# Optimization experiments

Hardware: AMD Instinct MI355X
Metric: run time of the kernel (lower is better)

Reference implementation:

```python
import jax, jax.numpy as jnp
import numpy as np

N_DEST, N_SRC = 8192, 8192
FEAT, TFD, EMB, HID, HEADS = 1024, 256, 64, 128, 2
NEG_INF = -9e15


def setup_inputs() -> dict:
    key = jax.random.key(0)
    ks = jax.random.split(key, 8)
    bias = (jax.random.uniform(ks[0], (N_DEST, N_SRC)) < 0.01).astype(jnp.float32)
    emb_dest = jax.random.normal(ks[1], (N_DEST, EMB), jnp.float32)
    emb_src = jax.random.normal(ks[2], (N_SRC, EMB), jnp.float32)
    feature_src = jax.random.normal(ks[3], (N_SRC, FEAT), jnp.float32)
    scale = 0.05
    fc_W = jax.random.normal(ks[4], (TFD, FEAT), jnp.float32) * scale
    fc_b = jnp.zeros((TFD,), jnp.float32)
    dec_W = jax.random.normal(ks[5], (FEAT, TFD), jnp.float32) * scale
    dec_b = jnp.zeros((FEAT,), jnp.float32)
    att_W = jax.random.normal(ks[6], (HEADS, EMB, HID), jnp.float32) * scale
    att_W2 = jax.random.normal(ks[7], (HEADS, HID, HID), jnp.float32) * scale
    return dict(bias=bias, emb_dest=emb_dest, emb_src=emb_src,
                feature_src=feature_src, fc_W=fc_W, fc_b=fc_b,
                dec_W=dec_W, dec_b=dec_b, att_W=att_W, att_W2=att_W2)


def reference(bias, emb_dest, emb_src, feature_src, fc_W, fc_b, dec_W, dec_b, att_W, att_W2):
    # encoder: [N_src, FEAT] -> [N_src, TFD]
    transformed = feature_src @ fc_W.T + fc_b
    # per-head projections of node embeddings: h = emb @ W  -> [H, N, HID]
    h_src = jnp.einsum('ne,hed->hnd', emb_src, att_W)
    h_dst = jnp.einsum('me,hed->hmd', emb_dest, att_W)
    # e = elu((h_dst @ W2) @ h_src^T)  -> [H, N_dest, N_src]
    scores = jax.nn.elu(jnp.einsum('hmd,hdk,hnk->hmn', h_dst, att_W2, h_src))
    masked = jnp.where(bias > 0, scores, NEG_INF)
    attn = jax.nn.softmax(masked, axis=-1)  # row-wise over source nodes
    # aggregate transformed source features, mean over heads -> [N_dest, TFD]
    feature_src_re = jnp.einsum('hmn,nf->hmf', attn, transformed).mean(axis=0)
    # decoder (autoencoder reconstruction): [N_src, FEAT]
    feature_hat = transformed @ dec_W.T + dec_b
    return feature_src_re, feature_hat
```

## Files before the change

### kernel.cpp

```cpp
#include <hip/hip_runtime.h>
#include <hip/hip_bf16.h>

#define N_DEST 8192
#define N_SRC  8192
#define FEATD  1024
#define TFDIM  256
#define EMBD   64
#define HIDD   128
#define LDO    1024
#define CAP 1024
#define LSTRIDE 256
#define SCAP 240

typedef float  f32x4  __attribute__((ext_vector_type(4)));
typedef __bf16 bf16x8 __attribute__((ext_vector_type(8)));
typedef unsigned short u16x4 __attribute__((ext_vector_type(4)));

__device__ inline bf16x8 load8cvt(const float* p) {
  const f32x4 u = *(const f32x4*)p;
  const f32x4 v = *(const f32x4*)(p + 4);
  bf16x8 r;
  #pragma unroll
  for (int i = 0; i < 4; ++i) { r[i] = (__bf16)u[i]; r[i + 4] = (__bf16)v[i]; }
  return r;
}
__device__ inline unsigned short bfbits(float f) {
  __bf16 b = (__bf16)f;
  return *(unsigned short*)&b;
}
__device__ inline float bf2f(unsigned short u) {
  union { unsigned int i; float f; } x;
  x.i = (unsigned int)u << 16;
  return x.f;
}

__global__ __launch_bounds__(256) void gemm_mfma_k1(
    const float* __restrict__ A, const float* __restrict__ B,
    const float* __restrict__ bias, float* __restrict__ stage,
    unsigned short* __restrict__ apack)
{
  const int wave = threadIdx.x >> 6, lane = threadIdx.x & 63;
  const int l15 = lane & 15, quad = lane >> 4;
  const int row0 = blockIdx.x * 64 + wave * 16;
  const int col0 = blockIdx.y * 64;

  const float* Ap = A + (size_t)(row0 + l15) * FEATD + quad * 8;
  const float* Bp = B + (size_t)(col0 + l15) * FEATD + quad * 8;

  f32x4 acc[4];
  #pragma unroll
  for (int i = 0; i < 4; ++i) acc[i] = (f32x4){0.f, 0.f, 0.f, 0.f};

  for (int k = 0; k < FEATD; k += 32) {
    const bf16x8 a  = load8cvt(Ap + k);
    const bf16x8 b0 = load8cvt(Bp + k);
    const bf16x8 b1 = load8cvt(Bp + (size_t)16 * FEATD + k);
    const bf16x8 b2 = load8cvt(Bp + (size_t)32 * FEATD + k);
    const bf16x8 b3 = load8cvt(Bp + (size_t)48 * FEATD + k);
    acc[0] = __builtin_amdgcn_mfma_f32_16x16x32_bf16(a, b0, acc[0], 0, 0, 0);
    acc[1] = __builtin_amdgcn_mfma_f32_16x16x32_bf16(a, b1, acc[1], 0, 0, 0);
    acc[2] = __builtin_amdgcn_mfma_f32_16x16x32_bf16(a, b2, acc[2], 0, 0, 0);
    acc[3] = __builtin_amdgcn_mfma_f32_16x16x32_bf16(a, b3, acc[3], 0, 0, 0);
  }

  #pragma unroll
  for (int ct = 0; ct < 4; ++ct) {
    const int n = col0 + ct * 16 + l15;
    const float bn = bias[n];
    #pragma unroll
    for (int r = 0; r < 4; ++r) {
      const int mm = row0 + quad * 4 + r;
      const float v = acc[ct][r] + bn;
      const unsigned short pb = bfbits(v);
      stage[(size_t)mm * LDO + n] = v;
      ((unsigned short*)(stage + (size_t)mm * LDO + 768))[n] = pb;
      if (apack) apack[(size_t)mm * TFDIM + n] = pb;
    }
  }
}

__global__ __launch_bounds__(128) void proj_all(
    const float* __restrict__ emb_src, const float* __restrict__ emb_dest,
    const float* __restrict__ att_W, const float* __restrict__ att_W2,
    float* __restrict__ stage)
{
  const int t = threadIdx.x;
  const int b = blockIdx.x;
  const int rb    = b & 511;
  const int h     = (b >> 9) & 1;
  const int which = b >> 10;
  const int row0  = rb * 16;

  __shared__ float se[16][EMBD];
  __shared__ float hh[16][HIDD];

  const float* e = (which ? emb_dest : emb_src) + (size_t)row0 * EMBD;
  for (int i = t; i < 16 * EMBD; i += 128) se[i >> 6][i & 63] = e[i];
  __syncthreads();

  float acc[16];
  #pragma unroll
  for (int r = 0; r < 16; ++r) acc[r] = 0.f;
  const float* W = att_W + (size_t)h * EMBD * HIDD + t;
  for (int d = 0; d < EMBD; ++d) {
    const float w = W[d * HIDD];
    #pragma unroll
    for (int r = 0; r < 16; ++r) acc[r] += se[r][d] * w;
  }

  if (!which) {
    #pragma unroll
    for (int r = 0; r < 16; ++r) {
      const size_t row = row0 + r;
      stage[row * LDO + 256 + h * HIDD + t] = acc[r];
      ((unsigned short*)(stage + row * LDO + 896))[h * HIDD + t] = bfbits(acc[r]);
    }
    return;
  }

  #pragma unroll
  for (int r = 0; r < 16; ++r) hh[r][t] = acc[r];
  __syncthreads();

  float g[16];
  #pragma unroll
  for (int r = 0; r < 16; ++r) g[r] = 0.f;
  const float* W2 = att_W2 + (size_t)h * HIDD * HIDD + t;
  for (int d = 0; d < HIDD; ++d) {
    const float w2 = W2[d * HIDD];
    #pragma unroll
    for (int r = 0; r < 16; ++r) g[r] += hh[r][d] * w2;
  }
  #pragma unroll
  for (int r = 0; r < 16; ++r)
    stage[(size_t)(row0 + r) * LDO + 512 + h * HIDD + t] = g[r];
}

__global__ __launch_bounds__(256) void extract_nbrs(
    const float* __restrict__ bias, int* __restrict__ counts,
    int* __restrict__ lists)
{
  const int m = blockIdx.x;
  __shared__ int cnt;
  __shared__ int buf[CAP];
  if (threadIdx.x == 0) cnt = 0;
  __syncthreads();
  const float* brow = bias + (size_t)m * N_SRC;
  for (int base = threadIdx.x * 4; base < N_SRC; base += 1024) {
    const f32x4 v = *(const f32x4*)(brow + base);
    #pragma unroll
    for (int e = 0; e < 4; ++e)
      if (v[e] > 0.f) {
        const int p = atomicAdd(&cnt, 1);
        if (p < CAP) buf[p] = base + e;
      }
  }
  __syncthreads();
  const int c = cnt;
  if (threadIdx.x == 0) counts[m] = c;
  int lim = c < LSTRIDE ? c : LSTRIDE;
  for (int t = threadIdx.x; t < lim; t += 256)
    lists[(size_t)m * LSTRIDE + t] = buf[t];
}

__global__ __launch_bounds__(256, 4) void attn_gather(
    const float* __restrict__ bias, const float* __restrict__ stage,
    const int* __restrict__ counts, const int* __restrict__ lists,
    float* __restrict__ out)
{
  const int m = blockIdx.x;
  const int tid = threadIdx.x;
  const int lane = tid & 63, wv = tid >> 6;

  __shared__ float g0[HIDD], g1[HIDD];
  __shared__ float s0[256], s1[256];
  __shared__ int   lidx[256];
  __shared__ float rA[4], rB[4];
  __shared__ float p0[4][TFDIM], p1[4][TFDIM];

  const float* gs = stage + (size_t)m * LDO + 512;
  if (tid < 128) { g0[tid] = gs[tid]; g1[tid] = gs[HIDD + tid]; }
  const int count = counts[m];
  __syncthreads();

  if (count > 0 && count <= SCAP) {
    const int countPad = (count + 15) & ~15;
    if (tid < countPad)
      lidx[tid] = (tid < count) ? lists[(size_t)m * LSTRIDE + tid] : 0;
    __syncthreads();

    const int grp = tid >> 3, r8 = tid & 7;
    for (int t0 = 0; t0 < count; t0 += 32) {
      const int t = t0 + grp;
      float q0 = 0.f, q1 = 0.f;
      if (t < count) {
        const int j = lidx[t];
        const __bf16* hb = (const __bf16*)(stage + (size_t)j * LDO + 896);
        const bf16x8 x0 = *(const bf16x8*)(hb + r8 * 16);
        const bf16x8 x1 = *(const bf16x8*)(hb + r8 * 16 + 8);
        const bf16x8 y0 = *(const bf16x8*)(hb + HIDD + r8 * 16);
        const bf16x8 y1 = *(const bf16x8*)(hb + HIDD + r8 * 16 + 8);
        #pragma unroll
        for (int e = 0; e < 8; ++e) {
          q0 += g0[r8 * 16 + e]     * (float)x0[e];
          q0 += g0[r8 * 16 + 8 + e] * (float)x1[e];
          q1 += g1[r8 * 16 + e]     * (float)y0[e];
          q1 += g1[r8 * 16 + 8 + e] * (float)y1[e];
        }
      }
      #pragma unroll
      for (int off = 1; off < 8; off <<= 1) {
        q0 += __shfl_xor(q0, off);
        q1 += __shfl_xor(q1, off);
      }
      if (r8 == 0 && t < count) {
        s0[t] = (q0 > 0.f) ? q0 : expm1f(q0);
        s1[t] = (q1 > 0.f) ? q1 : expm1f(q1);
      }
    }
    __syncthreads();

    float m0 = (tid < count) ? s0[tid] : -3.4e38f;
    float m1 = (tid < count) ? s1[tid] : -3.4e38f;
    #pragma unroll
    for (int off = 32; off; off >>= 1) {
      m0 = fmaxf(m0, __shfl_xor(m0, off));
      m1 = fmaxf(m1, __shfl_xor(m1, off));
    }
    if (lane == 0) { rA[wv] = m0; rB[wv] = m1; }
    __syncthreads();
    const float M0 = fmaxf(fmaxf(rA[0], rA[1]), fmaxf(rA[2], rA[3]));
    const float M1 = fmaxf(fmaxf(rB[0], rB[1]), fmaxf(rB[2], rB[3]));
    __syncthreads();

    float w0 = 0.f, w1 = 0.f;
    if (tid < count) {
      w0 = __expf(s0[tid] - M0);
      w1 = __expf(s1[tid] - M1);
    }
    if (tid < countPad) { s0[tid] = w0; s1[tid] = w1; }
    float l0 = w0, l1 = w1;
    #pragma unroll
    for (int off = 32; off; off >>= 1) {
      l0 += __shfl_xor(l0, off);
      l1 += __shfl_xor(l1, off);
    }
    if (lane == 0) { rA[wv] = l0; rB[wv] = l1; }
    __syncthreads();
    const float L0 = rA[0] + rA[1] + rA[2] + rA[3];
    const float L1 = rB[0] + rB[1] + rB[2] + rB[3];

    float b0[4] = {0.f, 0.f, 0.f, 0.f};
    float b1[4] = {0.f, 0.f, 0.f, 0.f};
    const int c4 = lane << 2;
    for (int t = wv << 2; t < countPad; t += 16) {
      #pragma unroll
      for (int q = 0; q < 4; ++q) {
        const int j = lidx[t + q];
        const float u0 = s0[t + q], u1 = s1[t + q];
        const u16x4 tv = *(const u16x4*)(
            (const unsigned short*)(stage + (size_t)j * LDO + 768) + c4);
        #pragma unroll
        for (int i = 0; i < 4; ++i) {
          const float f = bf2f(tv[i]);
          b0[i] += u0 * f;
          b1[i] += u1 * f;
        }
      }
    }
    #pragma unroll
    for (int i = 0; i < 4; ++i) {
      p0[wv][c4 + i] = b0[i];
      p1[wv][c4 + i] = b1[i];
    }
    __syncthreads();
    const float A0 = p0[0][tid] + p0[1][tid] + p0[2][tid] + p0[3][tid];
    const float A1 = p1[0][tid] + p1[1][tid] + p1[2][tid] + p1[3][tid];
    out[(size_t)m * TFDIM + tid] = 0.5f * (A0 / L0 + A1 / L1);
    return;
  }

  float* w0s = (float*)p0[0];
  float* w1s = (float*)p0[1];
  const int c = tid;
  float a0 = 0.f, a1 = 0.f;
  float M0 = -3.4e38f, M1 = -3.4e38f, L0 = 0.f, L1 = 0.f;
  for (int j0 = 0; j0 < N_SRC; j0 += 256) {
    const int j = j0 + tid;
    const float* hb = stage + (size_t)j * LDO + 256;
    float q0 = 0.f, q1 = 0.f;
    for (int d = 0; d < HIDD; d += 4) {
      const f32x4 x = *(const f32x4*)(hb + d);
      const f32x4 y = *(const f32x4*)(hb + HIDD + d);
      #pragma unroll
      for (int e = 0; e < 4; ++e) {
        q0 += g0[d + e] * x[e];
        q1 += g1[d + e] * y[e];
      }
    }
    const bool nz = bias[(size_t)m * N_SRC + j] > 0.f;
    const float sc0 = nz ? ((q0 > 0.f) ? q0 : expm1f(q0)) : -9e15f;
    const float sc1 = nz ? ((q1 > 0.f) ? q1 : expm1f(q1)) : -9e15f;

    float cm0 = sc0, cm1 = sc1;
    #pragma unroll
    for (int off = 32; off; off >>= 1) {
      cm0 = fmaxf(cm0, __shfl_xor(cm0, off));
      cm1 = fmaxf(cm1, __shfl_xor(cm1, off));
    }
    if (lane == 0) { rA[wv] = cm0; rB[wv] = cm1; }
    __syncthreads();
    const float CM0 = fmaxf(fmaxf(rA[0], rA[1]), fmaxf(rA[2], rA[3]));
    const float CM1 = fmaxf(fmaxf(rB[0], rB[1]), fmaxf(rB[2], rB[3]));
    __syncthreads();

    const float nM0 = fmaxf(M0, CM0), nM1 = fmaxf(M1, CM1);
    const float r0 = __expf(M0 - nM0), r1 = __expf(M1 - nM1);
    const float w0 = __expf(sc0 - nM0), w1 = __expf(sc1 - nM1);
    w0s[tid] = w0; w1s[tid] = w1;
    float cl0 = w0, cl1 = w1;
    #pragma unroll
    for (int off = 32; off; off >>= 1) {
      cl0 += __shfl_xor(cl0, off);
      cl1 += __shfl_xor(cl1, off);
    }
    if (lane == 0) { rA[wv] = cl0; rB[wv] = cl1; }
    __syncthreads();
    L0 = L0 * r0 + (rA[0] + rA[1] + rA[2] + rA[3]);
    L1 = L1 * r1 + (rB[0] + rB[1] + rB[2] + rB[3]);
    M0 = nM0; M1 = nM1;
    a0 *= r0; a1 *= r1;
    for (int t2 = 0; t2 < 256; ++t2) {
      const float tv = stage[(size_t)(j0 + t2) * LDO + c];
      a0 += w0s[t2] * tv;
      a1 += w1s[t2] * tv;
    }
    __syncthreads();
  }
  out[(size_t)m * TFDIM + c] = 0.5f * (a0 / L0 + a1 / L1);
}

__global__ __launch_bounds__(64) void attn_stream(
    const float* __restrict__ bias, const float* __restrict__ stage,
    float* __restrict__ out)
{
  const int lane = threadIdx.x;
  const int m = blockIdx.x;
  const int c0 = lane * 4;

  __shared__ float g0[HIDD], g1[HIDD];
  __shared__ int   ring[256];
  __shared__ float wb0[64], wb1[64];

  const float* gs = stage + (size_t)m * LDO + 512;
  g0[lane]      = gs[lane];
  g0[lane + 64] = gs[lane + 64];
  g1[lane]      = gs[HIDD + lane];
  g1[lane + 64] = gs[HIDD + lane + 64];
  __syncthreads();

  float O0[4] = {0.f, 0.f, 0.f, 0.f};
  float O1[4] = {0.f, 0.f, 0.f, 0.f};
  float M0 = -3.4e38f, M1 = -3.4e38f;
  float L0 = 0.f, L1 = 0.f;

  auto flush = [&](int b, int rp) {
    __syncthreads();
    int j = -1;
    if (lane < b) j = ring[(rp + lane) & 255];
    float s0 = 0.f, s1 = 0.f;
    if (j >= 0) {
      const float* h0 = stage + (size_t)j * LDO + 256;
      const float* h1 = h0 + HIDD;
      #pragma unroll
      for (int d = 0; d < HIDD; d += 4) {
        const f32x4 a = *(const f32x4*)(h0 + d);
        const f32x4 c = *(const f32x4*)(h1 + d);
        #pragma unroll
        for (int e = 0; e < 4; ++e) {
          s0 += g0[d + e] * a[e];
          s1 += g1[d + e] * c[e];
        }
      }
      s0 = (s0 > 0.f) ? s0 : expm1f(s0);
      s1 = (s1 > 0.f) ? s1 : expm1f(s1);
    }
    float m0 = (j >= 0) ? s0 : -3.4e38f;
    float m1 = (j >= 0) ? s1 : -3.4e38f;
    #pragma unroll
    for (int off = 32; off; off >>= 1) {
      m0 = fmaxf(m0, __shfl_xor(m0, off));
      m1 = fmaxf(m1, __shfl_xor(m1, off));
    }
    const float nM0 = fmaxf(M0, m0), nM1 = fmaxf(M1, m1);
    const float w0 = (j >= 0) ? __expf(s0 - nM0) : 0.f;
    const float w1 = (j >= 0) ? __expf(s1 - nM1) : 0.f;
    float l0 = w0, l1 = w1;
    #pragma unroll
    for (int off = 32; off; off >>= 1) {
      l0 += __shfl_xor(l0, off);
      l1 += __shfl_xor(l1, off);
    }
    const float r0 = __expf(M0 - nM0);
    const float r1 = __expf(M1 - nM1);
    L0 = L0 * r0 + l0;  L1 = L1 * r1 + l1;
    M0 = nM0;  M1 = nM1;
    #pragma unroll
    for (int i = 0; i < 4; ++i) { O0[i] *= r0; O1[i] *= r1; }
    wb0[lane] = w0;  wb1[lane] = w1;
    __syncthreads();
    for (int n = 0; n < b; ++n) {
      const int jj = ring[(rp + n) & 255];
      const float wa = wb0[n], wc = wb1[n];
      const f32x4 tv = *(const f32x4*)(stage + (size_t)jj * LDO + c0);
      #pragma unroll
      for (int i = 0; i < 4; ++i) {
        O0[i] += wa * tv[i];
        O1[i] += wc * tv[i];
      }
    }
    __syncthreads();
  };

  const float* brow = bias + (size_t)m * N_SRC;
  int wpos = 0, rpos = 0;
  for (int base = 0; base < N_SRC; base += 256) {
    const f32x4 v = *(const f32x4*)(brow + base + lane * 4);
    #pragma unroll
    for (int e = 0; e < 4; ++e) {
      const bool nz = v[e] > 0.f;
      const unsigned long long mask = __ballot(nz);
      if (nz) {
        const int pos = wpos + __popcll(mask & ((1ull << lane) - 1ull));
        ring[pos & 255] = base + lane * 4 + e;
      }
      wpos += __popcll(mask);
      if (wpos - rpos >= 64) { flush(64, rpos); rpos += 64; }
    }
  }
  while (wpos - rpos > 0) {
    const int b = (wpos - rpos < 64) ? (wpos - rpos) : 64;
    flush(b, rpos);
    rpos += b;
  }

  float* orow = out + (size_t)m * TFDIM + c0;
  if (wpos == 0) {
    float o[4] = {0.f, 0.f, 0.f, 0.f};
    for (int j = 0; j < N_SRC; ++j) {
      const f32x4 tv = *(const f32x4*)(stage + (size_t)j * LDO + c0);
      #pragma unroll
      for (int i = 0; i < 4; ++i) o[i] += tv[i];
    }
    const float inv = 1.f / (float)N_SRC;
    #pragma unroll
    for (int i = 0; i < 4; ++i) orow[i] = o[i] * inv;
  } else {
    const float i0 = 1.f / L0, i1 = 1.f / L1;
    #pragma unroll
    for (int i = 0; i < 4; ++i)
      orow[i] = 0.5f * (O0[i] * i0 + O1[i] * i1);
  }
}

__global__ __launch_bounds__(256) void gemm_mfma_dec2(
    const unsigned short* __restrict__ apack,
    const float* __restrict__ W,
    const float* __restrict__ bias,
    float* __restrict__ OUT)
{
  const int wave = threadIdx.x >> 6, lane = threadIdx.x & 63;
  const int l15 = lane & 15, quad = lane >> 4;
  const int row0 = blockIdx.x * 64 + wave * 16;
  const int col0 = blockIdx.y * 64;

  const unsigned short* Ap = apack + (size_t)(row0 + l15) * TFDIM + quad * 8;
  const float* Bp = W + (size_t)(col0 + l15) * TFDIM + quad * 8;

  f32x4 acc[4];
  #pragma unroll
  for (int i = 0; i < 4; ++i) acc[i] = (f32x4){0.f, 0.f, 0.f, 0.f};

  #pragma unroll
  for (int k = 0; k < TFDIM; k += 32) {
    const bf16x8 a  = *(const bf16x8*)(Ap + k);
    const bf16x8 b0 = load8cvt(Bp + k);
    const bf16x8 b1 = load8cvt(Bp + (size_t)16 * TFDIM + k);
    const bf16x8 b2 = load8cvt(Bp + (size_t)32 * TFDIM + k);
    const bf16x8 b3 = load8cvt(Bp + (size_t)48 * TFDIM + k);
    acc[0] = __builtin_amdgcn_mfma_f32_16x16x32_bf16(a, b0, acc[0], 0, 0, 0);
    acc[1] = __builtin_amdgcn_mfma_f32_16x16x32_bf16(a, b1, acc[1], 0, 0, 0);
    acc[2] = __builtin_amdgcn_mfma_f32_16x16x32_bf16(a, b2, acc[2], 0, 0, 0);
    acc[3] = __builtin_amdgcn_mfma_f32_16x16x32_bf16(a, b3, acc[3], 0, 0, 0);
  }

  #pragma unroll
  for (int ct = 0; ct < 4; ++ct) {
    const int n = col0 + ct * 16 + l15;
    const float bn = bias[n];
    #pragma unroll
    for (int r = 0; r < 4; ++r) {
      const int mm = row0 + quad * 4 + r;
      OUT[(size_t)mm * LDO + n] = acc[ct][r] + bn;
    }
  }
}

__global__ __launch_bounds__(128) void gemm_mfma_dec(
    const float* __restrict__ W,
    const float* __restrict__ bias,
    float* __restrict__ OUT)
{
  const int row0 = blockIdx.x * 32;
  const int tid = threadIdx.x;
  const int wave = tid >> 6, lane = tid & 63;
  const int l15 = lane & 15, quad = lane >> 4;

  __shared__ __bf16 Ab[32][TFDIM + 8];

  for (int i = tid; i < 32 * TFDIM; i += 128) {
    const int r = i >> 8, k = i & 255;
    Ab[r][k] = (__bf16)OUT[(size_t)(row0 + r) * LDO + k];
  }
  __syncthreads();

  bf16x8 af[8];
  #pragma unroll
  for (int ks = 0; ks < 8; ++ks)
    af[ks] = *(const bf16x8*)&Ab[wave * 16 + l15][ks * 32 + quad * 8];

  for (int ct = 0; ct < 16; ++ct) {
    f32x4 acc[4];
    #pragma unroll
    for (int i = 0; i < 4; ++i) acc[i] = (f32x4){0.f, 0.f, 0.f, 0.f};
    #pragma unroll
    for (int ks = 0; ks < 8; ++ks) {
      #pragma unroll
      for (int cg = 0; cg < 4; ++cg) {
        const int n = ct * 64 + cg * 16 + l15;
        const bf16x8 bf = load8cvt(W + (size_t)n * TFDIM + ks * 32 + quad * 8);
        acc[cg] = __builtin_amdgcn_mfma_f32_16x16x32_bf16(af[ks], bf, acc[cg], 0, 0, 0);
      }
    }
    #pragma unroll
    for (int cg = 0; cg < 4; ++cg) {
      const int n = ct * 64 + cg * 16 + l15;
      const float bn = bias[n];
      #pragma unroll
      for (int r = 0; r < 4; ++r) {
        const int mm = row0 + wave * 16 + quad * 4 + r;
        OUT[(size_t)mm * LDO + n] = acc[cg][r] + bn;
      }
    }
  }
}

extern "C" void kernel_launch(void* const* d_in, const int* in_sizes, int n_in,
                              void* d_out, int out_size, void* d_ws, size_t ws_size,
                              hipStream_t stream) {
  const float* bias        = (const float*)d_in[0];
  const float* emb_dest    = (const float*)d_in[1];
  const float* emb_src     = (const float*)d_in[2];
  const float* feature_src = (const float*)d_in[3];
  const float* fc_W        = (const float*)d_in[4];
  const float* fc_b        = (const float*)d_in[5];
  const float* dec_W       = (const float*)d_in[6];
  const float* dec_b       = (const float*)d_in[7];
  const float* att_W       = (const float*)d_in[8];
  const float* att_W2      = (const float*)d_in[9];

  float* out0 = (float*)d_out;
  float* out1 = out0 + (size_t)N_DEST * TFDIM;

  const size_t lists_bytes = (size_t)N_DEST * LSTRIDE * sizeof(int);
  const size_t apack_bytes = (size_t)N_SRC * TFDIM * sizeof(unsigned short);
  const size_t need = (size_t)65536 + lists_bytes + apack_bytes;
  const bool use_ws = (ws_size >= need);
  int* counts = (int*)d_ws;
  int* lists  = (int*)((char*)d_ws + 65536);
  unsigned short* apack =
      (unsigned short*)((char*)d_ws + 65536 + lists_bytes);

  {
    dim3 grid(N_SRC / 64, TFDIM / 64);
    gemm_mfma_k1<<<grid, 256, 0, stream>>>(feature_src, fc_W, fc_b, out1,
                                           use_ws ? apack : (unsigned short*)nullptr);
  }
  proj_all<<<2048, 128, 0, stream>>>(emb_src, emb_dest, att_W, att_W2, out1);
  if (use_ws) {
    extract_nbrs<<<N_DEST, 256, 0, stream>>>(bias, counts, lists);
    attn_gather<<<N_DEST, 256, 0, stream>>>(bias, out1, counts, lists, out0);
  } else {
    attn_stream<<<N_DEST, 64, 0, stream>>>(bias, out1, out0);
  }
  if (use_ws) {
    dim3 grid(N_SRC / 64, FEATD / 64);
    gemm_mfma_dec2<<<grid, 256, 0, stream>>>(apack, dec_W, dec_b, out1);
  } else {
    gemm_mfma_dec<<<N_SRC / 32, 128, 0, stream>>>(dec_W, dec_b, out1);
  }
}
```

Measured before the change: 692.3 us.

## Fuse neighbor extraction into attention kernel and pre-convert weights to bf16

Result: faster. 635.3 us (-8.2%).

```diff
diff --git a/kernel.cpp b/kernel.cpp
--- a/kernel.cpp
+++ b/kernel.cpp
@@ -8,8 +8,6 @@
 #define EMBD   64
 #define HIDD   128
 #define LDO    1024
-#define CAP 1024
-#define LSTRIDE 256
 #define SCAP 240
 
 typedef float  f32x4  __attribute__((ext_vector_type(4)));
@@ -34,10 +32,26 @@
   return x.f;
 }
 
+__global__ __launch_bounds__(256) void cvt_weights(
+    const float* __restrict__ fc_W, const float* __restrict__ dec_W,
+    unsigned short* __restrict__ wpack, unsigned short* __restrict__ dpack)
+{
+  const int which = blockIdx.x >> 8;
+  const int i = ((blockIdx.x & 255) * 256 + threadIdx.x) * 4;
+  const float* src = which ? dec_W : fc_W;
+  unsigned short* dst = which ? dpack : wpack;
+  const f32x4 v = *(const f32x4*)(src + i);
+  u16x4 o;
+  #pragma unroll
+  for (int e = 0; e < 4; ++e) o[e] = bfbits(v[e]);
+  *(u16x4*)(dst + i) = o;
+}
+
 __global__ __launch_bounds__(256) void gemm_mfma_k1(
     const float* __restrict__ A, const float* __restrict__ B,
     const float* __restrict__ bias, float* __restrict__ stage,
-    unsigned short* __restrict__ apack)
+    unsigned short* __restrict__ apack,
+    const unsigned short* __restrict__ wpack)
 {
   const int wave = threadIdx.x >> 6, lane = threadIdx.x & 63;
   const int l15 = lane & 15, quad = lane >> 4;
@@ -45,22 +59,37 @@
   const int col0 = blockIdx.y * 64;
 
   const float* Ap = A + (size_t)(row0 + l15) * FEATD + quad * 8;
-  const float* Bp = B + (size_t)(col0 + l15) * FEATD + quad * 8;
 
   f32x4 acc[4];
   #pragma unroll
   for (int i = 0; i < 4; ++i) acc[i] = (f32x4){0.f, 0.f, 0.f, 0.f};
 
-  for (int k = 0; k < FEATD; k += 32) {
-    const bf16x8 a  = load8cvt(Ap + k);
-    const bf16x8 b0 = load8cvt(Bp + k);
-    const bf16x8 b1 = load8cvt(Bp + (size_t)16 * FEATD + k);
-    const bf16x8 b2 = load8cvt(Bp + (size_t)32 * FEATD + k);
-    const bf16x8 b3 = load8cvt(Bp + (size_t)48 * FEATD + k);
-    acc[0] = __builtin_amdgcn_mfma_f32_16x16x32_bf16(a, b0, acc[0], 0, 0, 0);
-    acc[1] = __builtin_amdgcn_mfma_f32_16x16x32_bf16(a, b1, acc[1], 0, 0, 0);
-    acc[2] = __builtin_amdgcn_mfma_f32_16x16x32_bf16(a, b2, acc[2], 0, 0, 0);
-    acc[3] = __builtin_amdgcn_mfma_f32_16x16x32_bf16(a, b3, acc[3], 0, 0, 0);
+  if (wpack) {
+    const unsigned short* Bq = wpack + (size_t)(col0 + l15) * FEATD + quad * 8;
+    for (int k = 0; k < FEATD; k += 32) {
+      const bf16x8 a  = load8cvt(Ap + k);
+      const bf16x8 b0 = *(const bf16x8*)(Bq + k);
+      const bf16x8 b1 = *(const bf16x8*)(Bq + (size_t)16 * FEATD + k);
+      const bf16x8 b2 = *(const bf16x8*)(Bq + (size_t)32 * FEATD + k);
+      const bf16x8 b3 = *(const bf16x8*)(Bq + (size_t)48 * FEATD + k);
+      acc[0] = __builtin_amdgcn_mfma_f32_16x16x32_bf16(a, b0, acc[0], 0, 0, 0);
+      acc[1] = __builtin_amdgcn_mfma_f32_16x16x32_bf16(a, b1, acc[1], 0, 0, 0);
+      acc[2] = __builtin_amdgcn_mfma_f32_16x16x32_bf16(a, b2, acc[2], 0, 0, 0);
+      acc[3] = __builtin_amdgcn_mfma_f32_16x16x32_bf16(a, b3, acc[3], 0, 0, 0);
+    }
+  } else {
+    const float* Bp = B + (size_t)(col0 + l15) * FEATD + quad * 8;
+    for (int k = 0; k < FEATD; k += 32) {
+      const bf16x8 a  = load8cvt(Ap + k);
+      const bf16x8 b0 = load8cvt(Bp + k);
+      const bf16x8 b1 = load8cvt(Bp + (size_t)16 * FEATD + k);
+      const bf16x8 b2 = load8cvt(Bp + (size_t)32 * FEATD + k);
+      const bf16x8 b3 = load8cvt(Bp + (size_t)48 * FEATD + k);
+      acc[0] = __builtin_amdgcn_mfma_f32_16x16x32_bf16(a, b0, acc[0], 0, 0, 0);
+      acc[1] = __builtin_amdgcn_mfma_f32_16x16x32_bf16(a, b1, acc[1], 0, 0, 0);
+      acc[2] = __builtin_amdgcn_mfma_f32_16x16x32_bf16(a, b2, acc[2], 0, 0, 0);
+      acc[3] = __builtin_amdgcn_mfma_f32_16x16x32_bf16(a, b3, acc[3], 0, 0, 0);
+    }
   }
 
   #pragma unroll
@@ -136,36 +165,8 @@
     stage[(size_t)(row0 + r) * LDO + 512 + h * HIDD + t] = g[r];
 }
 
-__global__ __launch_bounds__(256) void extract_nbrs(
-    const float* __restrict__ bias, int* __restrict__ counts,
-    int* __restrict__ lists)
-{
-  const int m = blockIdx.x;
-  __shared__ int cnt;
-  __shared__ int buf[CAP];
-  if (threadIdx.x == 0) cnt = 0;
-  __syncthreads();
-  const float* brow = bias + (size_t)m * N_SRC;
-  for (int base = threadIdx.x * 4; base < N_SRC; base += 1024) {
-    const f32x4 v = *(const f32x4*)(brow + base);
-    #pragma unroll
-    for (int e = 0; e < 4; ++e)
-      if (v[e] > 0.f) {
-        const int p = atomicAdd(&cnt, 1);
-        if (p < CAP) buf[p] = base + e;
-      }
-  }
-  __syncthreads();
-  const int c = cnt;
-  if (threadIdx.x == 0) counts[m] = c;
-  int lim = c < LSTRIDE ? c : LSTRIDE;
-  for (int t = threadIdx.x; t < lim; t += 256)
-    lists[(size_t)m * LSTRIDE + t] = buf[t];
-}
-
-__global__ __launch_bounds__(256, 4) void attn_gather(
+__global__ __launch_bounds__(256, 4) void attn_fused(
     const float* __restrict__ bias, const float* __restrict__ stage,
-    const int* __restrict__ counts, const int* __restrict__ lists,
     float* __restrict__ out)
 {
   const int m = blockIdx.x;
@@ -177,45 +178,52 @@
   __shared__ int   lidx[256];
   __shared__ float rA[4], rB[4];
   __shared__ float p0[4][TFDIM], p1[4][TFDIM];
+  __shared__ int   cnt;
 
   const float* gs = stage + (size_t)m * LDO + 512;
   if (tid < 128) { g0[tid] = gs[tid]; g1[tid] = gs[HIDD + tid]; }
-  const int count = counts[m];
+  if (tid == 0) cnt = 0;
   __syncthreads();
+
+  const float* brow = bias + (size_t)m * N_SRC;
+  for (int base = tid * 4; base < N_SRC; base += 1024) {
+    const f32x4 v = *(const f32x4*)(brow + base);
+    #pragma unroll
+    for (int e = 0; e < 4; ++e)
+      if (v[e] > 0.f) {
+        const int p = atomicAdd(&cnt, 1);
+        if (p < 256) lidx[p] = base + e;
+      }
+  }
+  __syncthreads();
+  const int count = cnt;
 
   if (count > 0 && count <= SCAP) {
     const int countPad = (count + 15) & ~15;
-    if (tid < countPad)
-      lidx[tid] = (tid < count) ? lists[(size_t)m * LSTRIDE + tid] : 0;
-    __syncthreads();
-
-    const int grp = tid >> 3, r8 = tid & 7;
-    for (int t0 = 0; t0 < count; t0 += 32) {
+    if (tid >= count && tid < countPad) lidx[tid] = 0;
+    __syncthreads();
+
+    const int grp = tid >> 2, r4 = tid & 3;
+    const int h = r4 >> 1, half = r4 & 1;
+    const float* gh = (h ? g1 : g0) + half * 64;
+    for (int t0 = 0; t0 < count; t0 += 64) {
       const int t = t0 + grp;
-      float q0 = 0.f, q1 = 0.f;
+      float q = 0.f;
       if (t < count) {
         const int j = lidx[t];
-        const __bf16* hb = (const __bf16*)(stage + (size_t)j * LDO + 896);
-        const bf16x8 x0 = *(const bf16x8*)(hb + r8 * 16);
-        const bf16x8 x1 = *(const bf16x8*)(hb + r8 * 16 + 8);
-        const bf16x8 y0 = *(const bf16x8*)(hb + HIDD + r8 * 16);
-        const bf16x8 y1 = *(const bf16x8*)(hb + HIDD + r8 * 16 + 8);
+        const __bf16* hb =
+            (const __bf16*)(stage + (size_t)j * LDO + 896) + h * HIDD + half * 64;
         #pragma unroll
-        for (int e = 0; e < 8; ++e) {
-          q0 += g0[r8 * 16 + e]     * (float)x0[e];
-          q0 += g0[r8 * 16 + 8 + e] * (float)x1[e];
-          q1 += g1[r8 * 16 + e]     * (float)y0[e];
-          q1 += g1[r8 * 16 + 8 + e] * (float)y1[e];
+        for (int s = 0; s < 8; ++s) {
+          const bf16x8 x = *(const bf16x8*)(hb + s * 8);
+          #pragma unroll
+          for (int e = 0; e < 8; ++e) q += gh[s * 8 + e] * (float)x[e];
         }
       }
-      #pragma unroll
-      for (int off = 1; off < 8; off <<= 1) {
-        q0 += __shfl_xor(q0, off);
-        q1 += __shfl_xor(q1, off);
-      }
-      if (r8 == 0 && t < count) {
-        s0[t] = (q0 > 0.f) ? q0 : expm1f(q0);
-        s1[t] = (q1 > 0.f) ? q1 : expm1f(q1);
+      q += __shfl_xor(q, 1);
+      if (t < count && half == 0) {
+        const float sc = (q > 0.f) ? q : expm1f(q);
+        if (h == 0) s0[t] = sc; else s1[t] = sc;
       }
     }
     __syncthreads();
@@ -340,132 +348,9 @@
   out[(size_t)m * TFDIM + c] = 0.5f * (a0 / L0 + a1 / L1);
 }
 
-__global__ __launch_bounds__(64) void attn_stream(
-    const float* __restrict__ bias, const float* __restrict__ stage,
-    float* __restrict__ out)
-{
-  const int lane = threadIdx.x;
-  const int m = blockIdx.x;
-  const int c0 = lane * 4;
-
-  __shared__ float g0[HIDD], g1[HIDD];
-  __shared__ int   ring[256];
-  __shared__ float wb0[64], wb1[64];
-
-  const float* gs = stage + (size_t)m * LDO + 512;
-  g0[lane]      = gs[lane];
-  g0[lane + 64] = gs[lane + 64];
-  g1[lane]      = gs[HIDD + lane];
-  g1[lane + 64] = gs[HIDD + lane + 64];
-  __syncthreads();
-
-  float O0[4] = {0.f, 0.f, 0.f, 0.f};
-  float O1[4] = {0.f, 0.f, 0.f, 0.f};
-  float M0 = -3.4e38f, M1 = -3.4e38f;
-  float L0 = 0.f, L1 = 0.f;
-
-  auto flush = [&](int b, int rp) {
-    __syncthreads();
-    int j = -1;
-    if (lane < b) j = ring[(rp + lane) & 255];
-    float s0 = 0.f, s1 = 0.f;
-    if (j >= 0) {
-      const float* h0 = stage + (size_t)j * LDO + 256;
-      const float* h1 = h0 + HIDD;
-      #pragma unroll
-      for (int d = 0; d < HIDD; d += 4) {
-        const f32x4 a = *(const f32x4*)(h0 + d);
-        const f32x4 c = *(const f32x4*)(h1 + d);
-        #pragma unroll
-        for (int e = 0; e < 4; ++e) {
-          s0 += g0[d + e] * a[e];
-          s1 += g1[d + e] * c[e];
-        }
-      }
-      s0 = (s0 > 0.f) ? s0 : expm1f(s0);
-      s1 = (s1 > 0.f) ? s1 : expm1f(s1);
-    }
-    float m0 = (j >= 0) ? s0 : -3.4e38f;
-    float m1 = (j >= 0) ? s1 : -3.4e38f;
-    #pragma unroll
-    for (int off = 32; off; off >>= 1) {
-      m0 = fmaxf(m0, __shfl_xor(m0, off));
-      m1 = fmaxf(m1, __shfl_xor(m1, off));
-    }
-    const float nM0 = fmaxf(M0, m0), nM1 = fmaxf(M1, m1);
-    const float w0 = (j >= 0) ? __expf(s0 - nM0) : 0.f;
-    const float w1 = (j >= 0) ? __expf(s1 - nM1) : 0.f;
-    float l0 = w0, l1 = w1;
-    #pragma unroll
-    for (int off = 32; off; off >>= 1) {
-      l0 += __shfl_xor(l0, off);
-      l1 += __shfl_xor(l1, off);
-    }
-    const float r0 = __expf(M0 - nM0);
-    const float r1 = __expf(M1 - nM1);
-    L0 = L0 * r0 + l0;  L1 = L1 * r1 + l1;
-    M0 = nM0;  M1 = nM1;
-    #pragma unroll
-    for (int i = 0; i < 4; ++i) { O0[i] *= r0; O1[i] *= r1; }
-    wb0[lane] = w0;  wb1[lane] = w1;
-    __syncthreads();
-    for (int n = 0; n < b; ++n) {
-      const int jj = ring[(rp + n) & 255];
-      const float wa = wb0[n], wc = wb1[n];
-      const f32x4 tv = *(const f32x4*)(stage + (size_t)jj * LDO + c0);
-      #pragma unroll
-      for (int i = 0; i < 4; ++i) {
-        O0[i] += wa * tv[i];
-        O1[i] += wc * tv[i];
-      }
-    }
-    __syncthreads();
-  };
-
-  const float* brow = bias + (size_t)m * N_SRC;
-  int wpos = 0, rpos = 0;
-  for (int base = 0; base < N_SRC; base += 256) {
-    const f32x4 v = *(const f32x4*)(brow + base + lane * 4);
-    #pragma unroll
-    for (int e = 0; e < 4; ++e) {
-      const bool nz = v[e] > 0.f;
-      const unsigned long long mask = __ballot(nz);
-      if (nz) {
-        const int pos = wpos + __popcll(mask & ((1ull << lane) - 1ull));
-        ring[pos & 255] = base + lane * 4 + e;
-      }
-      wpos += __popcll(mask);
-      if (wpos - rpos >= 64) { flush(64, rpos); rpos += 64; }
-    }
-  }
-  while (wpos - rpos > 0) {
-    const int b = (wpos - rpos < 64) ? (wpos - rpos) : 64;
-    flush(b, rpos);
-    rpos += b;
-  }
-
-  float* orow = out + (size_t)m * TFDIM + c0;
-  if (wpos == 0) {
-    float o[4] = {0.f, 0.f, 0.f, 0.f};
-    for (int j = 0; j < N_SRC; ++j) {
-      const f32x4 tv = *(const f32x4*)(stage + (size_t)j * LDO + c0);
-      #pragma unroll
-      for (int i = 0; i < 4; ++i) o[i] += tv[i];
-    }
-    const float inv = 1.f / (float)N_SRC;
-    #pragma unroll
-    for (int i = 0; i < 4; ++i) orow[i] = o[i] * inv;
-  } else {
-    const float i0 = 1.f / L0, i1 = 1.f / L1;
-    #pragma unroll
-    for (int i = 0; i < 4; ++i)
-      orow[i] = 0.5f * (O0[i] * i0 + O1[i] * i1);
-  }
-}
-
 __global__ __launch_bounds__(256) void gemm_mfma_dec2(
     const unsigned short* __restrict__ apack,
-    const float* __restrict__ W,
+    const unsigned short* __restrict__ dpack,
     const float* __restrict__ bias,
     float* __restrict__ OUT)
 {
@@ -475,7 +360,7 @@
   const int col0 = blockIdx.y * 64;
 
   const unsigned short* Ap = apack + (size_t)(row0 + l15) * TFDIM + quad * 8;
-  const float* Bp = W + (size_t)(col0 + l15) * TFDIM + quad * 8;
+  const unsigned short* Bp = dpack + (size_t)(col0 + l15) * TFDIM + quad * 8;
 
   f32x4 acc[4];
   #pragma unroll
@@ -484,10 +369,10 @@
   #pragma unroll
   for (int k = 0; k < TFDIM; k += 32) {
     const bf16x8 a  = *(const bf16x8*)(Ap + k);
-    const bf16x8 b0 = load8cvt(Bp + k);
-    const bf16x8 b1 = load8cvt(Bp + (size_t)16 * TFDIM + k);
-    const bf16x8 b2 = load8cvt(Bp + (size_t)32 * TFDIM + k);
-    const bf16x8 b3 = load8cvt(Bp + (size_t)48 * TFDIM + k);
+    const bf16x8 b0 = *(const bf16x8*)(Bp + k);
+    const bf16x8 b1 = *(const bf16x8*)(Bp + (size_t)16 * TFDIM + k);
+    const bf16x8 b2 = *(const bf16x8*)(Bp + (size_t)32 * TFDIM + k);
+    const bf16x8 b3 = *(const bf16x8*)(Bp + (size_t)48 * TFDIM + k);
     acc[0] = __builtin_amdgcn_mfma_f32_16x16x32_bf16(a, b0, acc[0], 0, 0, 0);
     acc[1] = __builtin_amdgcn_mfma_f32_16x16x32_bf16(a, b1, acc[1], 0, 0, 0);
     acc[2] = __builtin_amdgcn_mfma_f32_16x16x32_bf16(a, b2, acc[2], 0, 0, 0);
@@ -572,30 +457,29 @@
   float* out0 = (float*)d_out;
   float* out1 = out0 + (size_t)N_DEST * TFDIM;
 
-  const size_t lists_bytes = (size_t)N_DEST * LSTRIDE * sizeof(int);
   const size_t apack_bytes = (size_t)N_SRC * TFDIM * sizeof(unsigned short);
-  const size_t need = (size_t)65536 + lists_bytes + apack_bytes;
-  const bool use_ws = (ws_size >= need);
-  int* counts = (int*)d_ws;
-  int* lists  = (int*)((char*)d_ws + 65536);
-  unsigned short* apack =
-      (unsigned short*)((char*)d_ws + 65536 + lists_bytes);
+  const size_t wpack_bytes = (size_t)TFDIM * FEATD * sizeof(unsigned short);
+  const size_t dpack_bytes = (size_t)FEATD * TFDIM * sizeof(unsigned short);
+  const bool use_ws = (ws_size >= apack_bytes + wpack_bytes + dpack_bytes);
+  unsigned short* apack = (unsigned short*)d_ws;
+  unsigned short* wpack = (unsigned short*)((char*)d_ws + apack_bytes);
+  unsigned short* dpack = (unsigned short*)((char*)d_ws + apack_bytes + wpack_bytes);
+
+  if (use_ws)
+    cvt_weights<<<512, 256, 0, stream>>>(fc_W, dec_W, wpack, dpack);
 
   {
     dim3 grid(N_SRC / 64, TFDIM / 64);
-    gemm_mfma_k1<<<grid, 256, 0, stream>>>(feature_src, fc_W, fc_b, out1,
-                                           use_ws ? apack : (unsigned short*)nullptr);
+    gemm_mfma_k1<<<grid, 256, 0, stream>>>(
+        feature_src, fc_W, fc_b, out1,
+        use_ws ? apack : (unsigned short*)nullptr,
+        use_ws ? wpack : (const unsigned short*)nullptr);
   }
   proj_all<<<2048, 128, 0, stream>>>(emb_src, emb_dest, att_W, att_W2, out1);
-  if (use_ws) {
-    extract_nbrs<<<N_DEST, 256, 0, stream>>>(bias, counts, lists);
-    attn_gather<<<N_DEST, 256, 0, stream>>>(bias, out1, counts, lists, out0);
-  } else {
-    attn_stream<<<N_DEST, 64, 0, stream>>>(bias, out1, out0);
-  }
+  attn_fused<<<N_DEST, 256, 0, stream>>>(bias, out1, out0);
   if (use_ws) {
     dim3 grid(N_SRC / 64, FEATD / 64);
-    gemm_mfma_dec2<<<grid, 256, 0, stream>>>(apack, dec_W, dec_b, out1);
+    gemm_mfma_dec2<<<grid, 256, 0, stream>>>(apack, dpack, dec_b, out1);
   } else {
     gemm_mfma_dec<<<N_SRC / 32, 128, 0, stream>>>(dec_W, dec_b, out1);
   }
```
